# Performance work log

Measured on AMD Instinct MI355X. Metric: run time of the kernel, lower is better.

## Reference

```python
import jax, jax.numpy as jnp
import numpy as np

MEM = 512
DT = 0.1


def setup_inputs() -> dict:
    key = jax.random.key(0)
    k = jax.random.split(key, 4)
    B, L, IN = 64, 1024, 128
    u = jax.random.normal(k[0], (B, L, IN), dtype=jnp.float32)
    h0 = jnp.zeros((2, B, MEM), dtype=jnp.float32)
    # Linear weights stored as (in, out) so y = x @ W + b; scaled like torch default init
    Wi = jax.random.normal(k[1], (IN, 6 * MEM), dtype=jnp.float32) / np.sqrt(IN)
    bi = jnp.zeros((6 * MEM,), dtype=jnp.float32)
    Wm = jax.random.normal(k[2], (MEM, 5 * MEM), dtype=jnp.float32) / np.sqrt(MEM)
    bm = jnp.zeros((5 * MEM,), dtype=jnp.float32)
    return {"u": u, "h0": h0, "Wi": Wi, "bi": bi, "Wm": Wm, "bm": bm}


def _forward(u, h0, Wi, bi, Wm, bm):
    dt = jnp.float32(DT)
    # Input embedding is state-independent: precompute for all timesteps.
    ie = jnp.einsum('bli,ih->blh', u, Wi) + bi          # [B, L, 6*MEM]
    ie = jnp.moveaxis(ie, 1, 0)                          # [L, B, 6*MEM] for scan

    def step(carry, ie_t):
        hf, hs = carry
        i_a, i_b, i_c, i_d, i_e, i_o = jnp.split(ie_t, 6, axis=-1)
        me = hf @ Wm + bm                                # [B, 5*MEM]
        m_a, m_b, m_c, m_d, m_e = jnp.split(me, 5, axis=-1)
        a = 1.0 + jnp.tanh(i_a + m_a)
        b = 1.5 * (1.0 + jnp.tanh(i_b + m_b))
        c = 3.0 * dt + (1.0 - 3.0 * dt) * jax.nn.sigmoid(i_c + m_c)
        d = 0.3 * dt * jax.nn.sigmoid(i_d + m_d)
        e = 1.0 + jax.nn.sigmoid(i_e + m_e)
        hfn = (1.0 - c) * hf + c * jnp.tanh(i_o + (a + b * hf * hf - hs) * hf)
        hsn = hs * (1.0 - d) + d * (e * hf) ** 4
        return (hfn, hsn), hfn

    (hf_last, _), hf_seq = jax.lax.scan(step, (h0[0], h0[1]), ie)
    h_t = jnp.moveaxis(hf_seq, 0, 1)                     # [B, L, MEM]
    return h_t, hf_last[:, None, :]                      # matches (cat(h_t), h_t[-1])


def reference(u, h0, Wi, bi, Wm, bm):
    return _forward(u, h0, Wi, bi, Wm, bm)
```

## Files before the change

kernel.cpp:

```cpp
#include <hip/hip_runtime.h>
#include <hip/hip_bf16.h>
#include <cstdint>
#include <cstddef>

#define NWG   256
#define NTH   512
#define LSTEP 1024
#define FAST_TRIES 256

typedef __attribute__((ext_vector_type(8))) short short8;
typedef __attribute__((ext_vector_type(4))) float f32x4;
typedef __attribute__((ext_vector_type(4))) unsigned int u32x4;
typedef __attribute__((ext_vector_type(2))) unsigned int u32x2;

__device__ __forceinline__ unsigned f2bf_bits(float x) {
  __hip_bfloat16 h = __float2bfloat16(x);
  return (unsigned)__builtin_bit_cast(unsigned short, h);
}
__device__ __forceinline__ float bfbits2f(unsigned b) {
  return __bfloat162float(__builtin_bit_cast(__hip_bfloat16, (unsigned short)b));
}
__device__ __forceinline__ float ftanh(float x) {
  const float ax = fminf(fabsf(x), 15.f);
  const float e  = __expf(-2.f * ax);
  const float t  = (1.f - e) / (1.f + e);
  return copysignf(t, x);
}
__device__ __forceinline__ float fsig(float x) {
  const float xx = fmaxf(fminf(x, 30.f), -30.f);
  return 1.f / (1.f + __expf(-xx));
}


__global__ void __launch_bounds__(NTH, 2)
fused_scan(const float* __restrict__ u, const float* __restrict__ h0,
           const float* __restrict__ Wi, const float* __restrict__ bi,
           const float* __restrict__ Wm, const float* __restrict__ bm,
           float* __restrict__ out,
           unsigned long long* __restrict__ stateFA,
           unsigned long long* __restrict__ stateFB,
           unsigned long long* __restrict__ stateSA,
           unsigned long long* __restrict__ stateSB,
           unsigned* __restrict__ xcctab)
{
  __shared__ float part_s[5120];
  __shared__ float ie_part[3072];
  __shared__ float hf_own[128];
  __shared__ float hs_own[128];
  __shared__ float bm_s[80];
  __shared__ float bi_s[96];

  const int wg   = blockIdx.x;
  const int bc   = wg & 7;
  const int jc   = wg >> 3;
  const int j0   = jc * 16;
  const int r0   = bc * 8;
  const int tid  = threadIdx.x;
  const int w    = tid >> 6;
  const int lane = tid & 63;
  const int colf = lane & 15;
  const int ksub = lane >> 4;
  const int rloc = lane & 7;

  unsigned my_xcc;
  asm volatile("s_getreg_b32 %0, hwreg(HW_REG_XCC_ID)" : "=s"(my_xcc));
  my_xcc &= 0xffu;
  if (tid == 0) {
    unsigned* tp = xcctab + wg;
    const unsigned v = 0x100u | my_xcc;
    asm volatile("global_store_dword %0, %1, off sc1" :: "v"(tp), "v"(v) : "memory");
  }

  if (tid < 80) bm_s[tid] = bm[(tid % 5) * 512 + j0 + tid / 5];
  if (tid >= 128 && tid < 224) {
    const int c = tid - 128;
    bi_s[c] = bi[(c % 6) * 512 + j0 + c / 6];
  }
  if (tid < 128) {
    const int r = tid >> 4, j16 = tid & 15;
    const float f = h0[(size_t)(r0 + r) * 512 + j0 + j16];
    const float s = h0[(size_t)32768 + (size_t)(r0 + r) * 512 + j0 + j16];
    hf_own[tid] = f;
    hs_own[tid] = s;
    const unsigned hb = f2bf_bits(f);
    const unsigned lb = f2bf_bits(f - bfbits2f(hb));
    u32x2 pr; pr[0] = hb | (lb << 16); pr[1] = 1u;
    const size_t eo = (size_t)(r0 + r) * 512 + j0 + j16;
    asm volatile("global_store_dwordx2 %0, %1, off"     :: "v"(stateFA + eo), "v"(pr) : "memory");
    asm volatile("global_store_dwordx2 %0, %1, off sc1" :: "v"(stateSA + eo), "v"(pr) : "memory");
  }

  bool fastmode;
  {
    unsigned pv = 0x100u | my_xcc;
    if (lane < 4) {
      const unsigned* tp = xcctab + bc + (w * 4 + lane) * 8;
      for (;;) {
        unsigned v;
        asm volatile("global_load_dword %0, %1, off sc1" : "=&v"(v) : "v"(tp) : "memory");
        asm volatile("s_waitcnt vmcnt(0)" ::: "memory");
        __builtin_amdgcn_sched_barrier(0);
        if (v & 0x100u) { pv = v; break; }
        __builtin_amdgcn_s_sleep(1);
      }
    }
    fastmode = __all((pv & 0xffu) == my_xcc);
  }

  short8 bh[5][2], bl[5][2];
  #pragma unroll
  for (int nt = 0; nt < 5; ++nt) {
    const int c = nt * 16 + colf;
    const int gcol = (c % 5) * 512 + j0 + c / 5;
    #pragma unroll
    for (int kt = 0; kt < 2; ++kt) {
      #pragma unroll
      for (int j = 0; j < 8; ++j) {
        const int kg = w * 64 + kt * 32 + ksub * 8 + j;
        const float wv = Wm[(size_t)kg * 2560 + gcol];
        const unsigned hb = f2bf_bits(wv);
        bh[nt][kt][j] = (short)hb;
        bl[nt][kt][j] = (short)f2bf_bits(wv - bfbits2f(hb));
      }
    }
  }
  const int iekc = w & 3;
  const int ienh = w >> 2;
  short8 bih[3], bil[3];
  #pragma unroll
  for (int nt = 0; nt < 3; ++nt) {
    const int c = (ienh * 3 + nt) * 16 + colf;
    const int gcol = (c % 6) * 512 + j0 + c / 6;
    #pragma unroll
    for (int j = 0; j < 8; ++j) {
      const int kg = iekc * 32 + ksub * 8 + j;
      const float wv = Wi[(size_t)kg * 3072 + gcol];
      const unsigned hb = f2bf_bits(wv);
      bih[nt][j] = (short)hb;
      bil[nt][j] = (short)f2bf_bits(wv - bfbits2f(hb));
    }
  }

  const float* ubase = u + (size_t)(r0 + rloc) * 131072 + iekc * 32 + ksub * 8;

  auto ie_math = [&](float4 xa_, float4 xb_) {
    const float xv[8] = {xa_.x, xa_.y, xa_.z, xa_.w, xb_.x, xb_.y, xb_.z, xb_.w};
    short8 ah, al;
    #pragma unroll
    for (int j = 0; j < 8; ++j) {
      const unsigned hb = f2bf_bits(xv[j]);
      ah[j] = (short)hb;
      al[j] = (short)f2bf_bits(xv[j] - bfbits2f(hb));
    }
    f32x4 acc[3];
    #pragma unroll
    for (int nt = 0; nt < 3; ++nt) { acc[nt][0]=0.f; acc[nt][1]=0.f; acc[nt][2]=0.f; acc[nt][3]=0.f; }
    #pragma unroll
    for (int nt = 0; nt < 3; ++nt) {
      acc[nt] = __builtin_amdgcn_mfma_f32_16x16x32_bf16(ah, bih[nt], acc[nt], 0, 0, 0);
      acc[nt] = __builtin_amdgcn_mfma_f32_16x16x32_bf16(ah, bil[nt], acc[nt], 0, 0, 0);
      acc[nt] = __builtin_amdgcn_mfma_f32_16x16x32_bf16(al, bih[nt], acc[nt], 0, 0, 0);
    }
    if (lane < 32) {
      const int rb = (lane >> 4) * 4;
      #pragma unroll
      for (int nt = 0; nt < 3; ++nt)
        #pragma unroll
        for (int i = 0; i < 4; ++i)
          ie_part[iekc * 768 + (rb + i) * 96 + (ienh * 3 + nt) * 16 + colf] = acc[nt][i];
    }
  };

  {
    const float4 xa0 = *(const float4*)ubase;
    const float4 xb0 = *(const float4*)(ubase + 4);
    ie_math(xa0, xb0);
  }

  const bool active = (lane & 8) == 0;

  for (int st = 0; st < LSTEP; ++st) {
    const unsigned long long* __restrict__ scurF = (st & 1) ? stateFB : stateFA;
    unsigned long long* __restrict__ snxtF       = (st & 1) ? stateFA : stateFB;
    const unsigned long long* __restrict__ scurS = (st & 1) ? stateSB : stateSA;
    unsigned long long* __restrict__ snxtS       = (st & 1) ? stateSA : stateSB;

    {
      const unsigned tag = (unsigned)(st + 1);
      const size_t eoff = (size_t)(r0 + rloc) * 512 + w * 64 + ksub * 8;
      u32x4 p0 = {0,0,0,0}, p1 = {0,0,0,0}, p2 = {0,0,0,0}, p3 = {0,0,0,0};
      u32x4 p4 = {0,0,0,0}, p5 = {0,0,0,0}, p6 = {0,0,0,0}, p7 = {0,0,0,0};
      if (active) {
#define READ8(PTR, FLAG, OKVAR)                                                                              \
        {                                                                                                    \
          asm volatile("global_load_dwordx4 %0, %1, off " FLAG            : "=&v"(p0) : "v"(PTR) : "memory"); \
          asm volatile("global_load_dwordx4 %0, %1, off offset:16 " FLAG  : "=&v"(p1) : "v"(PTR) : "memory"); \
          asm volatile("global_load_dwordx4 %0, %1, off offset:32 " FLAG  : "=&v"(p2) : "v"(PTR) : "memory"); \
          asm volatile("global_load_dwordx4 %0, %1, off offset:48 " FLAG  : "=&v"(p3) : "v"(PTR) : "memory"); \
          asm volatile("global_load_dwordx4 %0, %1, off offset:256 " FLAG : "=&v"(p4) : "v"(PTR) : "memory"); \
          asm volatile("global_load_dwordx4 %0, %1, off offset:272 " FLAG : "=&v"(p5) : "v"(PTR) : "memory"); \
          asm volatile("global_load_dwordx4 %0, %1, off offset:288 " FLAG : "=&v"(p6) : "v"(PTR) : "memory"); \
          asm volatile("global_load_dwordx4 %0, %1, off offset:304 " FLAG : "=&v"(p7) : "v"(PTR) : "memory"); \
          asm volatile("s_waitcnt vmcnt(0)" ::: "memory");                                                   \
          __builtin_amdgcn_sched_barrier(0);                            \
          OKVAR = p0[1] >= tag && p0[3] >= tag && p1[1] >= tag && p1[3] >= tag                               \
               && p2[1] >= tag && p2[3] >= tag && p3[1] >= tag && p3[3] >= tag                               \
               && p4[1] >= tag && p4[3] >= tag && p5[1] >= tag && p5[3] >= tag                               \
               && p6[1] >= tag && p6[3] >= tag && p7[1] >= tag && p7[3] >= tag;                              \
        }
        bool got = false;
        if (fastmode) {
          const unsigned long long* baseF = scurF + eoff;
          int tries = 0;
          bool ok;
          do {
            READ8(baseF, "nt", ok)
            if (__all(ok)) { got = true; break; }
          } while (++tries < FAST_TRIES);
          if (!got) fastmode = false;
        }
        if (!got) {
          const unsigned long long* baseS = scurS + eoff;
          for (;;) {
            bool ok;
            READ8(baseS, "sc1", ok)
            if (__all(ok)) break;
            __builtin_amdgcn_s_sleep(1);
          }
        }
#undef READ8
      }
      __builtin_amdgcn_sched_barrier(0);
      short8 ah[2], al[2];
      ah[0][0] = (short)(p0[0] & 0xffffu); al[0][0] = (short)(p0[0] >> 16);
      ah[0][1] = (short)(p0[2] & 0xffffu); al[0][1] = (short)(p0[2] >> 16);
      ah[0][2] = (short)(p1[0] & 0xffffu); al[0][2] = (short)(p1[0] >> 16);
      ah[0][3] = (short)(p1[2] & 0xffffu); al[0][3] = (short)(p1[2] >> 16);
      ah[0][4] = (short)(p2[0] & 0xffffu); al[0][4] = (short)(p2[0] >> 16);
      ah[0][5] = (short)(p2[2] & 0xffffu); al[0][5] = (short)(p2[2] >> 16);
      ah[0][6] = (short)(p3[0] & 0xffffu); al[0][6] = (short)(p3[0] >> 16);
      ah[0][7] = (short)(p3[2] & 0xffffu); al[0][7] = (short)(p3[2] >> 16);
      ah[1][0] = (short)(p4[0] & 0xffffu); al[1][0] = (short)(p4[0] >> 16);
      ah[1][1] = (short)(p4[2] & 0xffffu); al[1][1] = (short)(p4[2] >> 16);
      ah[1][2] = (short)(p5[0] & 0xffffu); al[1][2] = (short)(p5[0] >> 16);
      ah[1][3] = (short)(p5[2] & 0xffffu); al[1][3] = (short)(p5[2] >> 16);
      ah[1][4] = (short)(p6[0] & 0xffffu); al[1][4] = (short)(p6[0] >> 16);
      ah[1][5] = (short)(p6[2] & 0xffffu); al[1][5] = (short)(p6[2] >> 16);
      ah[1][6] = (short)(p7[0] & 0xffffu); al[1][6] = (short)(p7[0] >> 16);
      ah[1][7] = (short)(p7[2] & 0xffffu); al[1][7] = (short)(p7[2] >> 16);
      f32x4 acc[5];
      #pragma unroll
      for (int nt = 0; nt < 5; ++nt) { acc[nt][0]=0.f; acc[nt][1]=0.f; acc[nt][2]=0.f; acc[nt][3]=0.f; }
      #pragma unroll
      for (int nt = 0; nt < 5; ++nt)
        #pragma unroll
        for (int kt = 0; kt < 2; ++kt) {
          acc[nt] = __builtin_amdgcn_mfma_f32_16x16x32_bf16(ah[kt], bh[nt][kt], acc[nt], 0, 0, 0);
          acc[nt] = __builtin_amdgcn_mfma_f32_16x16x32_bf16(ah[kt], bl[nt][kt], acc[nt], 0, 0, 0);
          acc[nt] = __builtin_amdgcn_mfma_f32_16x16x32_bf16(al[kt], bh[nt][kt], acc[nt], 0, 0, 0);
        }
      if (lane < 32) {
        const int rb = (lane >> 4) * 4;
        #pragma unroll
        for (int nt = 0; nt < 5; ++nt)
          #pragma unroll
          for (int i = 0; i < 4; ++i)
            part_s[(w * 8 + rb + i) * 80 + nt * 16 + colf] = acc[nt][i];
      }
    }
    __syncthreads();

    float4 xa = {0.f, 0.f, 0.f, 0.f}, xb = {0.f, 0.f, 0.f, 0.f};
    if (st + 1 < LSTEP) {
      const float* up = ubase + (size_t)(st + 1) * 128;
      xa = *(const float4*)up;
      xb = *(const float4*)(up + 4);
    }

    if (tid < 128) {
      const int r = tid >> 4, j16 = tid & 15;
      float m[5];
      #pragma unroll
      for (int g = 0; g < 5; ++g) {
        float v = bm_s[j16 * 5 + g];
        #pragma unroll
        for (int kh = 0; kh < 8; ++kh) v += part_s[kh * 640 + r * 80 + j16 * 5 + g];
        m[g] = v;
      }
      float iacc[6];
      #pragma unroll
      for (int g = 0; g < 6; ++g) {
        float v = bi_s[j16 * 6 + g];
        #pragma unroll
        for (int kc = 0; kc < 4; ++kc) v += ie_part[kc * 768 + r * 96 + j16 * 6 + g];
        iacc[g] = v;
      }
      const float hf = hf_own[tid];
      const float hs = hs_own[tid];
      const float a = 1.f + ftanh(iacc[0] + m[0]);
      const float b = 1.5f * (1.f + ftanh(iacc[1] + m[1]));
      const float c = 0.3f + 0.7f * fsig(iacc[2] + m[2]);
      const float d = 0.03f * fsig(iacc[3] + m[3]);
      const float e = 1.f + fsig(iacc[4] + m[4]);
      const float hfn_v = (1.f - c) * hf + c * ftanh(iacc[5] + (a + b * hf * hf - hs) * hf);
      const float eh  = e * hf;
      const float eh2 = eh * eh;
      const float hsn_v = hs * (1.f - d) + d * eh2 * eh2;
      hf_own[tid] = hfn_v;
      hs_own[tid] = hsn_v;
      const unsigned hb = f2bf_bits(hfn_v);
      const unsigned lb = f2bf_bits(hfn_v - bfbits2f(hb));
      u32x2 pr; pr[0] = hb | (lb << 16); pr[1] = (unsigned)(st + 2);
      const size_t eo = (size_t)(r0 + r) * 512 + j0 + j16;
      asm volatile("global_store_dwordx2 %0, %1, off"     :: "v"(snxtF + eo), "v"(pr) : "memory");
      asm volatile("global_store_dwordx2 %0, %1, off sc1" :: "v"(snxtS + eo), "v"(pr) : "memory");
      out[(size_t)(r0 + r) * 524288 + (size_t)st * 512 + j0 + j16] = hfn_v;
      if (st == LSTEP - 1)
        out[(size_t)33554432 + (size_t)(r0 + r) * 512 + j0 + j16] = hfn_v;
    }
    __syncthreads();
    if (st + 1 < LSTEP) ie_math(xa, xb);
  }
}

extern "C" void kernel_launch(void* const* d_in, const int* in_sizes, int n_in,
                              void* d_out, int out_size, void* d_ws, size_t ws_size,
                              hipStream_t stream) {
  (void)in_sizes; (void)n_in; (void)out_size; (void)ws_size;
  const float* u  = (const float*)d_in[0];
  const float* h0 = (const float*)d_in[1];
  const float* Wi = (const float*)d_in[2];
  const float* bi = (const float*)d_in[3];
  const float* Wm = (const float*)d_in[4];
  const float* bm = (const float*)d_in[5];
  float* out = (float*)d_out;
  unsigned* xcctab = (unsigned*)d_ws;
  char* sb = (char*)d_ws + 4096;
  unsigned long long* stateFA = (unsigned long long*)(sb);
  unsigned long long* stateFB = (unsigned long long*)(sb + 262144);
  unsigned long long* stateSA = (unsigned long long*)(sb + 2 * 262144);
  unsigned long long* stateSB = (unsigned long long*)(sb + 3 * 262144);
  hipMemsetAsync(d_ws, 0, 4096 + 4 * 262144, stream);
  hipLaunchKernelGGL(fused_scan, dim3(NWG), dim3(NTH), 0, stream,
                     u, h0, Wi, bi, Wm, bm, out,
                     stateFA, stateFB, stateSA, stateSB, xcctab);
}
```

Measured before the change: 2.902 ms.

## Double-buffer LDS partials to drop a barrier and spread the pointwise update across waves

Double-buffers the part_s and ie_part shared arrays by step parity, which lets the second __syncthreads per step be removed. The input-embedding MFMA for the current step now runs before the barrier instead of after the previous update. The pointwise recurrence update moves from threads 0-127 (two waves) to lanes 0-15 of each of the eight waves, so every wave does a slice of the epilogue. The aim is to shorten the serial critical path of each scan step, at the cost of twice the LDS and more idle lanes per wave.

```diff
diff --git a/kernel.cpp b/kernel.cpp
--- a/kernel.cpp
+++ b/kernel.cpp
@@ -43,8 +43,8 @@
            unsigned long long* __restrict__ stateSB,
            unsigned* __restrict__ xcctab)
 {
-  __shared__ float part_s[5120];
-  __shared__ float ie_part[3072];
+  __shared__ float part_s[2 * 5120];
+  __shared__ float ie_part[2 * 3072];
   __shared__ float hf_own[128];
   __shared__ float hs_own[128];
   __shared__ float bm_s[80];
@@ -143,7 +143,7 @@
 
   const float* ubase = u + (size_t)(r0 + rloc) * 131072 + iekc * 32 + ksub * 8;
 
-  auto ie_math = [&](float4 xa_, float4 xb_) {
+  auto ie_math = [&](float* iep, float4 xa_, float4 xb_) {
     const float xv[8] = {xa_.x, xa_.y, xa_.z, xa_.w, xb_.x, xb_.y, xb_.z, xb_.w};
     short8 ah, al;
     #pragma unroll
@@ -167,23 +167,22 @@
       for (int nt = 0; nt < 3; ++nt)
         #pragma unroll
         for (int i = 0; i < 4; ++i)
-          ie_part[iekc * 768 + (rb + i) * 96 + (ienh * 3 + nt) * 16 + colf] = acc[nt][i];
+          iep[iekc * 768 + (rb + i) * 96 + (ienh * 3 + nt) * 16 + colf] = acc[nt][i];
     }
   };
 
-  {
-    const float4 xa0 = *(const float4*)ubase;
-    const float4 xb0 = *(const float4*)(ubase + 4);
-    ie_math(xa0, xb0);
-  }
-
   const bool active = (lane & 8) == 0;
+  float4 xa = *(const float4*)ubase;
+  float4 xb = *(const float4*)(ubase + 4);
 
   for (int st = 0; st < LSTEP; ++st) {
-    const unsigned long long* __restrict__ scurF = (st & 1) ? stateFB : stateFA;
-    unsigned long long* __restrict__ snxtF       = (st & 1) ? stateFA : stateFB;
-    const unsigned long long* __restrict__ scurS = (st & 1) ? stateSB : stateSA;
-    unsigned long long* __restrict__ snxtS       = (st & 1) ? stateSA : stateSB;
+    const int pbit = st & 1;
+    const unsigned long long* __restrict__ scurF = pbit ? stateFB : stateFA;
+    unsigned long long* __restrict__ snxtF       = pbit ? stateFA : stateFB;
+    const unsigned long long* __restrict__ scurS = pbit ? stateSB : stateSA;
+    unsigned long long* __restrict__ snxtS       = pbit ? stateSA : stateSB;
+    float* psp = part_s  + pbit * 5120;
+    float* iep = ie_part + pbit * 3072;
 
     {
       const unsigned tag = (unsigned)(st + 1);
@@ -265,26 +264,25 @@
         for (int nt = 0; nt < 5; ++nt)
           #pragma unroll
           for (int i = 0; i < 4; ++i)
-            part_s[(w * 8 + rb + i) * 80 + nt * 16 + colf] = acc[nt][i];
-      }
-    }
-    __syncthreads();
-
-    float4 xa = {0.f, 0.f, 0.f, 0.f}, xb = {0.f, 0.f, 0.f, 0.f};
+            psp[(w * 8 + rb + i) * 80 + nt * 16 + colf] = acc[nt][i];
+      }
+    }
+    ie_math(iep, xa, xb);
     if (st + 1 < LSTEP) {
       const float* up = ubase + (size_t)(st + 1) * 128;
       xa = *(const float4*)up;
       xb = *(const float4*)(up + 4);
     }
-
-    if (tid < 128) {
-      const int r = tid >> 4, j16 = tid & 15;
+    __syncthreads();
+
+    if (lane < 16) {
+      const int j16 = lane;
       float m[5];
       #pragma unroll
       for (int g = 0; g < 5; ++g) {
         float v = bm_s[j16 * 5 + g];
         #pragma unroll
-        for (int kh = 0; kh < 8; ++kh) v += part_s[kh * 640 + r * 80 + j16 * 5 + g];
+        for (int kh = 0; kh < 8; ++kh) v += psp[kh * 640 + w * 80 + j16 * 5 + g];
         m[g] = v;
       }
       float iacc[6];
@@ -292,11 +290,12 @@
       for (int g = 0; g < 6; ++g) {
         float v = bi_s[j16 * 6 + g];
         #pragma unroll
-        for (int kc = 0; kc < 4; ++kc) v += ie_part[kc * 768 + r * 96 + j16 * 6 + g];
+        for (int kc = 0; kc < 4; ++kc) v += iep[kc * 768 + w * 96 + j16 * 6 + g];
         iacc[g] = v;
       }
-      const float hf = hf_own[tid];
-      const float hs = hs_own[tid];
+      const int hidx = w * 16 + j16;
+      const float hf = hf_own[hidx];
+      const float hs = hs_own[hidx];
       const float a = 1.f + ftanh(iacc[0] + m[0]);
       const float b = 1.5f * (1.f + ftanh(iacc[1] + m[1]));
       const float c = 0.3f + 0.7f * fsig(iacc[2] + m[2]);
@@ -306,20 +305,18 @@
       const float eh  = e * hf;
       const float eh2 = eh * eh;
       const float hsn_v = hs * (1.f - d) + d * eh2 * eh2;
-      hf_own[tid] = hfn_v;
-      hs_own[tid] = hsn_v;
+      hf_own[hidx] = hfn_v;
+      hs_own[hidx] = hsn_v;
       const unsigned hb = f2bf_bits(hfn_v);
       const unsigned lb = f2bf_bits(hfn_v - bfbits2f(hb));
       u32x2 pr; pr[0] = hb | (lb << 16); pr[1] = (unsigned)(st + 2);
-      const size_t eo = (size_t)(r0 + r) * 512 + j0 + j16;
+      const size_t eo = (size_t)(r0 + w) * 512 + j0 + j16;
       asm volatile("global_store_dwordx2 %0, %1, off"     :: "v"(snxtF + eo), "v"(pr) : "memory");
       asm volatile("global_store_dwordx2 %0, %1, off sc1" :: "v"(snxtS + eo), "v"(pr) : "memory");
-      out[(size_t)(r0 + r) * 524288 + (size_t)st * 512 + j0 + j16] = hfn_v;
+      out[(size_t)(r0 + w) * 524288 + (size_t)st * 512 + j0 + j16] = hfn_v;
       if (st == LSTEP - 1)
-        out[(size_t)33554432 + (size_t)(r0 + r) * 512 + j0 + j16] = hfn_v;
-    }
-    __syncthreads();
-    if (st + 1 < LSTEP) ie_math(xa, xb);
+        out[(size_t)33554432 + (size_t)(r0 + w) * 512 + j0 + j16] = hfn_v;
+    }
   }
 }
 
```

New measurement: 4.069 ms. 1.4x slower.
